# Optimization experiments

Hardware: AMD Instinct MI355X
Metric: run time of the kernel (lower is better)

The kernel has to match this reference:

```python
import jax, jax.numpy as jnp
import numpy as np

N_NODES = 8192
N_PAIRS = 524288
MAX_PATH = 5
D_FEAT = 128


def setup_inputs() -> dict:
    key = jax.random.key(0)
    k_x, k_b, k_src, k_dst, k_len = jax.random.split(key, 5)
    x = jax.random.normal(k_x, (N_NODES, D_FEAT), dtype=jnp.float32)
    b = jax.random.normal(k_b, (MAX_PATH,), dtype=jnp.float32)
    src = jax.random.randint(k_src, (N_PAIRS,), 0, N_NODES, dtype=jnp.int32)
    dst = jax.random.randint(k_dst, (N_PAIRS,), 0, N_NODES, dtype=jnp.int32)
    path_len = jax.random.randint(k_len, (N_PAIRS,), 0, 10, dtype=jnp.int32)
    return {"x": x, "b": b, "src": src, "dst": dst, "path_len": path_len}


def reference(x, b, src, dst, path_len):
    # bucket index = min(len(path), max_path_distance) - 1, clipped into [0, MAX_PATH-1]
    bucket = jnp.clip(jnp.minimum(path_len, MAX_PATH) - 1, 0, MAX_PATH - 1)
    vals = b[bucket]  # [n_pairs] gather from tiny bias table
    num_nodes = x.shape[0]
    spatial_matrix = jnp.zeros((num_nodes, num_nodes), dtype=jnp.float32)
    # single batched scatter replaces the per-edge python loop
    spatial_matrix = spatial_matrix.at[src, dst].set(vals)
    return spatial_matrix
```

## Files before the change

kernel.cpp:

```cpp
#include <hip/hip_runtime.h>


#define N_NODES   8192
#define N_PAIRS   524288
#define MAX_PATH  5
#define NTHR      256
#define PER_THR   4

__device__ __forceinline__ int bucket_of(int pl) {
    int b = min(pl, MAX_PATH) - 1;
    return max(0, min(b, MAX_PATH - 1));
}

__global__ __launch_bounds__(NTHR) void scatter_pass(
        const int4* __restrict__ src4,
        const int4* __restrict__ dst4,
        const int4* __restrict__ plen4,
        int* out_i) {
    const int t = blockIdx.x * NTHR + threadIdx.x;
    const int4 s = src4[t];
    const int4 d = dst4[t];
    const int4 p = plen4[t];
    const int base = t * PER_THR;

    const int cell0 = s.x * N_NODES + d.x;
    const int cell1 = s.y * N_NODES + d.y;
    const int cell2 = s.z * N_NODES + d.z;
    const int cell3 = s.w * N_NODES + d.w;

    atomicMax(&out_i[cell0], ((base + 1) << 3) | bucket_of(p.x));
    atomicMax(&out_i[cell1], ((base + 2) << 3) | bucket_of(p.y));
    atomicMax(&out_i[cell2], ((base + 3) << 3) | bucket_of(p.z));
    atomicMax(&out_i[cell3], ((base + 4) << 3) | bucket_of(p.w));
}

__global__ __launch_bounds__(NTHR) void resolve_pass(
        const int4* __restrict__ src4,
        const int4* __restrict__ dst4,
        const float* __restrict__ b,
        int* out_i,
        float* out_f) {
    const int t = blockIdx.x * NTHR + threadIdx.x;
    const int4 s = src4[t];
    const int4 d = dst4[t];
    const int base = t * PER_THR;

    const int cell[PER_THR] = { s.x * N_NODES + d.x, s.y * N_NODES + d.y,
                                s.z * N_NODES + d.z, s.w * N_NODES + d.w };
    #pragma unroll
    for (int k = 0; k < PER_THR; ++k) {
        const int cur = out_i[cell[k]];
        if ((cur >> 3) == base + k + 1) {
            __builtin_nontemporal_store(b[cur & 7], &out_f[cell[k]]);
        }
    }
}

extern "C" void kernel_launch(void* const* d_in, const int* in_sizes, int n_in,
                              void* d_out, int out_size, void* d_ws, size_t ws_size,
                              hipStream_t stream) {
    const float* b    = (const float*)d_in[1];
    const int4* src4  = (const int4*)d_in[2];
    const int4* dst4  = (const int4*)d_in[3];
    const int4* plen4 = (const int4*)d_in[4];

    float* out_f = (float*)d_out;
    int*   out_i = (int*)d_out;

    const int blocks = N_PAIRS / (NTHR * PER_THR);

    scatter_pass<<<blocks, NTHR, 0, stream>>>(src4, dst4, plen4, out_i);
    resolve_pass<<<blocks, NTHR, 0, stream>>>(src4, dst4, b, out_i, out_f);
}
```

Before: 313.8 us.

## Resolve duplicate scatter writes through a compact hash table instead of output atomics

Scatter-pass atomics now go to a 1M-entry open-addressing hash table in workspace, keyed by cell with the pair priority and bucket packed into 64 bits. They no longer hit the 256 MB output matrix directly. The resolve pass probes the table to find the winning pair per cell and writes only the winners. The aim is to keep the random atomics inside a small, cache-resident 8 MB table rather than spreading them across the huge output. The cost is an extra memset, CAS/probe loops and 64-bit atomics.

```diff
diff --git a/kernel.cpp b/kernel.cpp
--- a/kernel.cpp
+++ b/kernel.cpp
@@ -6,40 +6,66 @@
 #define MAX_PATH  5
 #define NTHR      256
 #define PER_THR   4
+#define TBITS     20
+#define TSIZE     (1u << TBITS)
+#define TMASK     (TSIZE - 1u)
+
+typedef unsigned long long u64;
 
 __device__ __forceinline__ int bucket_of(int pl) {
     int b = min(pl, MAX_PATH) - 1;
     return max(0, min(b, MAX_PATH - 1));
 }
 
+__device__ __forceinline__ unsigned hash_cell(int cell) {
+    return ((unsigned)cell * 2654435761u) >> (32 - TBITS);
+}
+
+__device__ __forceinline__ u64 pack_entry(int cell, int pri, int bkt) {
+    return ((u64)(unsigned)pri << 29) | ((u64)(unsigned)cell << 3) | (unsigned)bkt;
+}
+
+__device__ __forceinline__ void table_insert(u64* T, int cell, int pri, int bkt) {
+    unsigned h = hash_cell(cell);
+    const u64 me = pack_entry(cell, pri, bkt);
+    while (true) {
+        u64 e = __hip_atomic_load(&T[h], __ATOMIC_RELAXED, __HIP_MEMORY_SCOPE_AGENT);
+        if (e == 0ull) {
+            u64 old = atomicCAS(&T[h], 0ull, me);
+            if (old == 0ull) return;
+            e = old;
+        }
+        if (((e >> 3) & 0x3FFFFFFull) == (u64)(unsigned)cell) {
+            atomicMax(&T[h], me);
+            return;
+        }
+        h = (h + 1) & TMASK;
+    }
+}
+
 __global__ __launch_bounds__(NTHR) void scatter_pass(
         const int4* __restrict__ src4,
         const int4* __restrict__ dst4,
         const int4* __restrict__ plen4,
-        int* out_i) {
+        u64* __restrict__ T) {
     const int t = blockIdx.x * NTHR + threadIdx.x;
     const int4 s = src4[t];
     const int4 d = dst4[t];
     const int4 p = plen4[t];
     const int base = t * PER_THR;
 
-    const int cell0 = s.x * N_NODES + d.x;
-    const int cell1 = s.y * N_NODES + d.y;
-    const int cell2 = s.z * N_NODES + d.z;
-    const int cell3 = s.w * N_NODES + d.w;
-
-    atomicMax(&out_i[cell0], ((base + 1) << 3) | bucket_of(p.x));
-    atomicMax(&out_i[cell1], ((base + 2) << 3) | bucket_of(p.y));
-    atomicMax(&out_i[cell2], ((base + 3) << 3) | bucket_of(p.z));
-    atomicMax(&out_i[cell3], ((base + 4) << 3) | bucket_of(p.w));
+    table_insert(T, s.x * N_NODES + d.x, base + 1, bucket_of(p.x));
+    table_insert(T, s.y * N_NODES + d.y, base + 2, bucket_of(p.y));
+    table_insert(T, s.z * N_NODES + d.z, base + 3, bucket_of(p.z));
+    table_insert(T, s.w * N_NODES + d.w, base + 4, bucket_of(p.w));
 }
 
 __global__ __launch_bounds__(NTHR) void resolve_pass(
         const int4* __restrict__ src4,
         const int4* __restrict__ dst4,
         const float* __restrict__ b,
-        int* out_i,
-        float* out_f) {
+        const u64* __restrict__ T,
+        float* __restrict__ out_f) {
     const int t = blockIdx.x * NTHR + threadIdx.x;
     const int4 s = src4[t];
     const int4 d = dst4[t];
@@ -49,9 +75,16 @@
                                 s.z * N_NODES + d.z, s.w * N_NODES + d.w };
     #pragma unroll
     for (int k = 0; k < PER_THR; ++k) {
-        const int cur = out_i[cell[k]];
-        if ((cur >> 3) == base + k + 1) {
-            __builtin_nontemporal_store(b[cur & 7], &out_f[cell[k]]);
+        unsigned h = hash_cell(cell[k]);
+        u64 e;
+        while (true) {
+            e = T[h];
+            if (e != 0ull &&
+                ((e >> 3) & 0x3FFFFFFull) == (u64)(unsigned)cell[k]) break;
+            h = (h + 1) & TMASK;
+        }
+        if ((int)(e >> 29) == base + k + 1) {
+            __builtin_nontemporal_store(b[e & 7], &out_f[cell[k]]);
         }
     }
 }
@@ -65,10 +98,12 @@
     const int4* plen4 = (const int4*)d_in[4];
 
     float* out_f = (float*)d_out;
-    int*   out_i = (int*)d_out;
+    u64*   T     = (u64*)d_ws;
+
+    hipMemsetAsync(d_ws, 0, (size_t)TSIZE * sizeof(u64), stream);
 
     const int blocks = N_PAIRS / (NTHR * PER_THR);
 
-    scatter_pass<<<blocks, NTHR, 0, stream>>>(src4, dst4, plen4, out_i);
-    resolve_pass<<<blocks, NTHR, 0, stream>>>(src4, dst4, b, out_i, out_f);
+    scatter_pass<<<blocks, NTHR, 0, stream>>>(src4, dst4, plen4, T);
+    resolve_pass<<<blocks, NTHR, 0, stream>>>(src4, dst4, b, T, out_f);
 }
```

Measured after the change: 307.7 us. No clear change (-2.0%).
